# Optimization experiments

Measured on AMD Instinct MI355X. Metric: run time of the kernel, lower is better.

## Reference

```python
import jax, jax.numpy as jnp
import numpy as np
import math

B, S, L, K, NSTEPS = 32, 128, 4096, 129, 10
PAD = K // 2  # torch: int(kernel.shape[-1]/2)


def _grouped_xcorr(x, w):
    # torch F.conv1d semantics (cross-correlation), groups = channels
    # x: [B,C,L] f32, w: [C,1,K] f32 -> [B,C,L]
    return jax.lax.conv_general_dilated(
        x, w, window_strides=(1,), padding=[(PAD, PAD)],
        dimension_numbers=('NCH', 'OIH', 'NCH'), feature_group_count=x.shape[1])


def _matched_filter(x_re, x_im, k_re, k_im):
    # complex grouped conv with conj(kernel) repeated per pulse
    wc_re = jnp.tile(k_re[None, None, :], (S, 1, 1))
    wc_im = jnp.tile(-k_im[None, None, :], (S, 1, 1))  # conj
    out_re = _grouped_xcorr(x_re, wc_re) - _grouped_xcorr(x_im, wc_im)
    out_im = _grouped_xcorr(x_re, wc_im) + _grouped_xcorr(x_im, wc_re)
    return out_re + 1j * out_im  # complex64 [B,S,L]


def _produce_rd(x, w_mag, w_phase):
    phase = jnp.arctan(w_phase)                    # [B,S]
    norm_mag = S * jax.nn.softmax(w_mag, axis=-1)  # [B,S]
    iq = (norm_mag * jnp.exp(-1j * phase))[..., None] * x
    return jnp.fft.fftshift(jnp.fft.fft(iq, axis=-2), axes=-2)


def _circular_weighted_mean(w):
    # circular weighted mean of index over last axis; returns (magnitude, index)
    N = w.shape[-1]
    ang = (2.0 * jnp.pi / N) * jnp.arange(N, dtype=w.dtype)
    z = jnp.sum(w * jnp.exp(1j * ang), axis=-1)
    return jnp.abs(z), jnp.angle(z) / (2.0 * jnp.pi) * N


def _snr(rd):
    Bn, nfft, Ln = rd.shape
    e = jnp.abs(rd) ** 2                                   # [B,S,L]
    flat_idx = jnp.argmax(e.reshape(Bn, -1), axis=1)
    max_range = flat_idx % Ln                              # [B] (indices: constant wrt grad)
    col = jnp.take_along_axis(e, max_range[:, None, None], axis=2)[..., 0]  # [B,S]
    _, peak_idx = _circular_weighted_mean(col)
    # torch rounds + casts to int -> detached index
    idx = jax.lax.stop_gradient(jnp.round(peak_idx)).astype(jnp.int32) % nfft
    peak = jnp.take_along_axis(col, idx[:, None], axis=1)[:, 0]
    noise = (jnp.sum(col, axis=-1) - peak) / (nfft - 1)
    return 10.0 * jnp.log10(peak) - 10.0 * jnp.log10(noise)


def setup_inputs() -> dict:
    key = jax.random.key(0)
    ks = jax.random.split(key, 5)
    return {
        'x_re': jax.random.normal(ks[0], (B, S, L), jnp.float32),
        'x_im': jax.random.normal(ks[1], (B, S, L), jnp.float32),
        'kernel_re': jax.random.normal(ks[2], (K,), jnp.float32),
        'kernel_im': jax.random.normal(ks[3], (K,), jnp.float32),
        'log_step_mag': -2.0 * jnp.ones((S, NSTEPS), jnp.float32),
        'log_step_phase': -2.0 * jnp.ones((S, NSTEPS), jnp.float32),
        'w_phase_init': jax.random.uniform(ks[4], (B, S), jnp.float32),
    }


def reference(x_re, x_im, kernel_re, kernel_im, log_step_mag, log_step_phase, w_phase_init):
    x = _matched_filter(x_re, x_im, kernel_re, kernel_im)  # [B,S,L] complex64
    w_mag = jnp.ones((B, S), jnp.float32)
    w_phase = w_phase_init

    def loss_sum(wm, wp):
        return jnp.sum(_snr(_produce_rd(x, wm, wp)))

    grad_fn = jax.grad(loss_sum, argnums=(0, 1))
    ln10 = math.log(10.0)
    for i in range(NSTEPS):
        # torch detaches w_mag/w_phase before the inner autograd.grad
        g_mag, g_phase = grad_fn(jax.lax.stop_gradient(w_mag),
                                 jax.lax.stop_gradient(w_phase))
        lr_mag = jnp.exp(log_step_mag[:, i] * ln10)    # 10**log_step
        lr_phase = jnp.exp(log_step_phase[:, i] * ln10)
        w_mag = w_mag + lr_mag * g_mag
        w_phase = w_phase + lr_phase * g_phase
    return jnp.mean(_snr(_produce_rd(x, w_mag, w_phase)))
```

## Files before the change

### kernel.cpp

```cpp
#include <hip/hip_runtime.h>

#define BB 32
#define SS 128
#define LL 4096
#define KK 129
#define NST 10

constexpr double PI_D = 3.141592653589793238462643383279502884;
constexpr double red_sin(double x){
  double x2 = x*x, t = x, r = x;
  t *= -x2/6.0;   r += t;
  t *= -x2/20.0;  r += t;
  t *= -x2/42.0;  r += t;
  t *= -x2/72.0;  r += t;
  t *= -x2/110.0; r += t;
  t *= -x2/156.0; r += t;
  t *= -x2/210.0; r += t;
  t *= -x2/272.0; r += t;
  return r;
}
constexpr double csin_d(double x){
  while (x >  PI_D) x -= 2.0*PI_D;
  while (x < -PI_D) x += 2.0*PI_D;
  if (x >  PI_D*0.5)      x =  PI_D - x;
  else if (x < -PI_D*0.5) x = -PI_D - x;
  return red_sin(x);
}
constexpr double ccos_d(double x){ return csin_d(x + PI_D*0.5); }
struct TWT { float c[64]; float s[64]; };
constexpr TWT make_tw(){
  TWT t{};
  for (int j = 0; j < 64; j++){
    double a = -2.0*PI_D*(double)j/128.0;
    t.c[j] = (float)ccos_d(a);
    t.s[j] = (float)csin_d(a);
  }
  return t;
}
constexpr TWT TW = make_tw();

#define PHYS8(i) ((i) + ((i) >> 3))

__global__ __launch_bounds__(256) void mf_kernel(const float* __restrict__ xr,
                                                 const float* __restrict__ xi,
                                                 const float* __restrict__ kr,
                                                 const float* __restrict__ ki,
                                                 float2* __restrict__ out)
{
  const int row = blockIdx.x >> 1;
  const int l0  = (blockIdx.x & 1) * 2048;
  const int t   = threadIdx.x;
  __shared__ float2 xs[2456];
  __shared__ float2 ks[132];
  if (t < KK) ks[t] = make_float2(kr[t], ki[t]);

  const float* xrr = xr + (size_t)row*LL;
  const float* xir = xi + (size_t)row*LL;
  for (int i4 = t; i4 < 544; i4 += 256){
    const int g0 = l0 - 64 + i4*4;
    float4 a, c;
    if (g0 >= 0 && g0 + 3 < LL){
      a = *(const float4*)(xrr + g0);
      c = *(const float4*)(xir + g0);
    } else {
      float av[4], cv[4];
      #pragma unroll
      for (int e = 0; e < 4; ++e){
        const int g = g0 + e;
        const bool ok = (g >= 0 && g < LL);
        av[e] = ok ? xrr[g] : 0.0f;
        cv[e] = ok ? xir[g] : 0.0f;
      }
      a = make_float4(av[0],av[1],av[2],av[3]);
      c = make_float4(cv[0],cv[1],cv[2],cv[3]);
    }
    const int i = i4*4;
    const int p = PHYS8(i);
    xs[p]   = make_float2(a.x, c.x);
    xs[p+1] = make_float2(a.y, c.y);
    xs[p+2] = make_float2(a.z, c.z);
    xs[p+3] = make_float2(a.w, c.w);
  }
  __syncthreads();

  const int base_l = t*8;
  float wr_[16], wi_[16];
  #pragma unroll
  for (int v = 0; v < 12; v += 2){
    const float4 p = *(const float4*)(&xs[PHYS8(base_l + v)]);
    wr_[v]   = p.x; wi_[v]   = p.y;
    wr_[v+1] = p.z; wi_[v+1] = p.w;
  }

  float2 acc[8];
  #pragma unroll
  for (int j = 0; j < 8; j++) acc[j] = make_float2(0.0f, 0.0f);

  #pragma unroll 1
  for (int q8 = 0; q8 < 8; ++q8){
    #pragma unroll
    for (int qq = 0; qq < 4; ++qq){
      const int q = q8*4 + qq;
      float4 p0, p1;
      const bool doref = (q < 31);
      if (doref){
        const int v0 = base_l + q*4 + 12;
        p0 = *(const float4*)(&xs[PHYS8(v0)]);
        p1 = *(const float4*)(&xs[PHYS8(v0 + 2)]);
      }
      float2 wv[4];
      #pragma unroll
      for (int kk = 0; kk < 4; ++kk) wv[kk] = ks[q*4 + kk];
      #pragma unroll
      for (int kk = 0; kk < 4; ++kk){
        const float wx = wv[kk].x, wy = wv[kk].y;
        #pragma unroll
        for (int j = 0; j < 8; ++j){
          const int sl = (qq*4 + kk + j) & 15;
          const float xvr = wr_[sl], xvi = wi_[sl];
          acc[j].x = fmaf(xvr, wx, acc[j].x);
          acc[j].x = fmaf(xvi, wy, acc[j].x);
          acc[j].y = fmaf(xvi, wx, acc[j].y);
          acc[j].y = fmaf(-xvr, wy, acc[j].y);
        }
      }
      if (doref){
        const int s0 = (qq*4 + 12) & 15;
        wr_[s0]   = p0.x; wi_[s0]   = p0.y;
        wr_[s0+1] = p0.z; wi_[s0+1] = p0.w;
        wr_[s0+2] = p1.x; wi_[s0+2] = p1.y;
        wr_[s0+3] = p1.z; wi_[s0+3] = p1.w;
      }
    }
  }
  {
    const float2 w = ks[128];
    #pragma unroll
    for (int j = 0; j < 8; ++j){
      const float xvr = wr_[j], xvi = wi_[j];
      acc[j].x = fmaf(xvr, w.x, acc[j].x);
      acc[j].x = fmaf(xvi, w.y, acc[j].x);
      acc[j].y = fmaf(xvi, w.x, acc[j].y);
      acc[j].y = fmaf(-xvr, w.y, acc[j].y);
    }
  }

  float4* orow = (float4*)(out + (size_t)row*LL + l0 + base_l);
  #pragma unroll
  for (int q = 0; q < 4; ++q){
    orow[q] = make_float4(acc[2*q].x, acc[2*q].y, acc[2*q+1].x, acc[2*q+1].y);
  }
}

__global__ __launch_bounds__(512) void tr_kernel(const float2* __restrict__ xmf,
                                                 float2* __restrict__ xt)
{
  const int b = blockIdx.y;
  const int l0 = blockIdx.x * 64;
  const int tid = threadIdx.x;
  __shared__ float ldr[64][129];
  __shared__ float ldi[64][129];
  #pragma unroll
  for (int it = 0; it < 8; ++it){
    const int flat = it*512 + tid;
    const int s  = flat >> 5;
    const int c4 = flat & 31;
    const float4 p = *(const float4*)(xmf + ((size_t)(b*SS + s))*LL + l0 + 2*c4);
    ldr[2*c4][s]   = p.x;  ldi[2*c4][s]   = p.y;
    ldr[2*c4+1][s] = p.z;  ldi[2*c4+1][s] = p.w;
  }
  __syncthreads();
  #pragma unroll
  for (int it = 0; it < 8; ++it){
    const int flat = it*512 + tid;
    const int dl = flat >> 6;
    const int s4 = flat & 63;
    const float r0 = ldr[dl][2*s4], r1 = ldr[dl][2*s4+1];
    const float i0 = ldi[dl][2*s4], i1 = ldi[dl][2*s4+1];
    *(float4*)(xt + ((size_t)b*LL + l0 + dl)*SS + 2*s4) = make_float4(r0, i0, r1, i1);
  }
}

__global__ void init_kernel(const float* __restrict__ wpi,
                            float* __restrict__ w_mag, float* __restrict__ w_phase,
                            float2* __restrict__ cvec, unsigned long long* __restrict__ slots,
                            float* __restrict__ out)
{
  const int i = blockIdx.x*256 + threadIdx.x;
  if (i < BB*SS){
    float wp = wpi[i];
    w_mag[i] = 1.0f;
    w_phase[i] = wp;
    float phi = atanf(wp);
    float s, c;
    sincosf(phi, &s, &c);
    cvec[i] = make_float2(c, -s);
  }
  if (i < BB) slots[i] = 0ull;
  if (i == 0) out[0] = 0.0f;
}

template<int SPAN, int N>
__device__ __forceinline__ void fstage(float2* v){
  #pragma unroll
  for (int b0 = 0; b0 < N; b0 += 2*SPAN){
    #pragma unroll
    for (int j = 0; j < SPAN; j++){
      const int i0 = b0 + j, i1 = b0 + j + SPAN;
      float ax = v[i0].x, ay = v[i0].y, bx = v[i1].x, by = v[i1].y;
      float sx = ax - bx, sy = ay - by;
      v[i0].x = ax + bx; v[i0].y = ay + by;
      const int tj = j * (64 / SPAN);
      if (tj == 0){
        v[i1].x = sx; v[i1].y = sy;
      } else if (tj == 32){
        v[i1].x = sy; v[i1].y = -sx;
      } else {
        const float wr = TW.c[tj], wi = TW.s[tj];
        v[i1].x = sx*wr - sy*wi;
        v[i1].y = sy*wr + sx*wi;
      }
    }
  }
}

__device__ __forceinline__ void scan_fft_tail(float2* v, int r, int tid, int l,
                                              unsigned long long* wred, int nwave,
                                              unsigned long long* slot)
{
  {
    const bool hi = (r & 2) != 0;
    const float sgn = hi ? -1.0f : 1.0f;
    const bool odd = (r & 1) != 0;
    #pragma unroll
    for (int j = 0; j < 32; ++j){
      float px = __shfl_xor(v[j].x, 2);
      float py = __shfl_xor(v[j].y, 2);
      float ux = fmaf(sgn, v[j].x, px);
      float uy = fmaf(sgn, v[j].y, py);
      float wr = hi ? (odd ? TW.s[j] : TW.c[j]) : 1.0f;
      float wi = hi ? (odd ? -TW.c[j] : TW.s[j]) : 0.0f;
      v[j].x = ux*wr - uy*wi;
      v[j].y = uy*wr + ux*wi;
    }
  }
  {
    const bool hi = (r & 1) != 0;
    const float sgn = hi ? -1.0f : 1.0f;
    #pragma unroll
    for (int j = 0; j < 32; ++j){
      float px = __shfl_xor(v[j].x, 1);
      float py = __shfl_xor(v[j].y, 1);
      float ux = fmaf(sgn, v[j].x, px);
      float uy = fmaf(sgn, v[j].y, py);
      float wr = hi ? TW.c[2*j] : 1.0f;
      float wi = hi ? TW.s[2*j] : 0.0f;
      v[j].x = ux*wr - uy*wi;
      v[j].y = uy*wr + ux*wi;
    }
  }
  fstage<16,32>(v); fstage<8,32>(v); fstage<4,32>(v); fstage<2,32>(v); fstage<1,32>(v);

  float mm = 0.0f;
  #pragma unroll
  for (int j = 0; j < 32; ++j) mm = fmaxf(mm, v[j].x*v[j].x + v[j].y*v[j].y);
  mm = fmaxf(mm, __shfl_xor(mm, 1));
  mm = fmaxf(mm, __shfl_xor(mm, 2));

  unsigned long long pk = ((unsigned long long)__float_as_uint(mm) << 32) | (unsigned int)l;
  #pragma unroll
  for (int m = 4; m < 64; m <<= 1){
    unsigned long long o = __shfl_xor(pk, m);
    if (o > pk) pk = o;
  }
  if ((tid & 63) == 0) wred[tid >> 6] = pk;
  __syncthreads();
  if (tid == 0){
    unsigned long long best = wred[0];
    for (int w = 1; w < nwave; ++w) if (wred[w] > best) best = wred[w];
    atomicMax(slot, best);
  }
}

__global__ __launch_bounds__(256) void scan_t_kernel(const float2* __restrict__ xt,
                                                     const float2* __restrict__ cvec,
                                                     unsigned long long* __restrict__ slots)
{
  const int b = blockIdx.y;
  const int tid = threadIdx.x;
  const int f = tid >> 2, r = tid & 3;
  const int l = blockIdx.x*64 + f;
  __shared__ float2 csh[SS];
  __shared__ unsigned long long wred[4];
  if (tid < SS) csh[tid] = cvec[b*SS + tid];
  __syncthreads();

  const float2* col = xt + ((size_t)b*LL + l)*SS + r*32;
  float2 v[32];
  #pragma unroll
  for (int i = 0; i < 8; ++i){
    const float4 p = ((const float4*)col)[i];
    v[2*i]   = make_float2(p.x, p.y);
    v[2*i+1] = make_float2(p.z, p.w);
  }
  #pragma unroll
  for (int j = 0; j < 32; ++j){
    const float2 c = csh[r*32 + j];
    const float2 x = v[j];
    v[j].x = c.x*x.x - c.y*x.y;
    v[j].y = c.x*x.y + c.y*x.x;
  }
  scan_fft_tail(v, r, tid, l, wred, 4, slots + b);
}

__global__ __launch_bounds__(512, 4) void scan_o_kernel(const float2* __restrict__ xmf,
                                                        const float2* __restrict__ cvec,
                                                        unsigned long long* __restrict__ slots)
{
  const int b = blockIdx.y;
  const int tid = threadIdx.x;
  const int l0 = blockIdx.x * 128;
  __shared__ float2 csh[SS];
  __shared__ float2 xsh[64][130];
  __shared__ unsigned long long wred[8];
  if (tid < SS) csh[tid] = cvec[b*SS + tid];

  const int f = tid >> 2, r = tid & 3;
  float2 v[32];

  #pragma unroll 1
  for (int h = 0; h < 2; ++h){
    __syncthreads();
    const float2* src = xmf + ((size_t)(b*SS + h*64))*LL + l0;
    #pragma unroll
    for (int it = 0; it < 8; ++it){
      const int flat = it*512 + tid;
      const int s1 = flat >> 6;
      const int c4 = flat & 63;
      const float4 vv = *(const float4*)(src + (size_t)s1*LL + c4*2);
      *(float4*)(&xsh[s1][c4*2]) = vv;
    }
    __syncthreads();
    if ((r >> 1) == h){
      #pragma unroll
      for (int j = 0; j < 32; ++j){
        const int rowi = (r & 1)*32 + j;
        const float2 x = xsh[rowi][f];
        const float2 c = csh[r*32 + j];
        v[j].x = c.x*x.x - c.y*x.y;
        v[j].y = c.x*x.y + c.y*x.x;
      }
    }
  }
  scan_fft_tail(v, r, tid, l0 + f, wred, 8, slots + b);
}

__device__ __forceinline__ float wredsum(float v){
  #pragma unroll
  for (int m = 1; m < 64; m <<= 1) v += __shfl_xor(v, m);
  return v;
}
__device__ __forceinline__ float wredmax(float v){
  #pragma unroll
  for (int m = 1; m < 64; m <<= 1) v = fmaxf(v, __shfl_xor(v, m));
  return v;
}
__device__ __forceinline__ float bsum256(float v, float* red4, int t){
  v = wredsum(v);
  __syncthreads();
  if ((t & 63) == 0) red4[t >> 6] = v;
  __syncthreads();
  return red4[0] + red4[1] + red4[2] + red4[3];
}
__device__ __forceinline__ float bmax256(float v, float* red4, int t){
  v = wredmax(v);
  __syncthreads();
  if ((t & 63) == 0) red4[t >> 6] = v;
  __syncthreads();
  return fmaxf(fmaxf(red4[0], red4[1]), fmaxf(red4[2], red4[3]));
}

__global__ __launch_bounds__(256) void step_kernel(const float2* __restrict__ xmf,
                                                   const float2* __restrict__ xt, int useT,
                                                   float* __restrict__ w_mag,
                                                   float* __restrict__ w_phase,
                                                   float2* __restrict__ cvec,
                                                   unsigned long long* __restrict__ slots,
                                                   const float* __restrict__ lsm,
                                                   const float* __restrict__ lsp,
                                                   int stepi, int isFinal,
                                                   float* __restrict__ out)
{
  const int b = blockIdx.x, t = threadIdx.x;
  const int s = t >> 1, h = t & 1;
  __shared__ float2 ysh[SS];
  __shared__ float twc[SS], tws[SS];
  __shared__ float red4[4];
  __shared__ float speak;
  __shared__ int sidx;

  const int rbin = (int)(slots[b] & 0xffffffffull);
  const float wm0 = w_mag[b*SS + s];
  const float wp0 = w_phase[b*SS + s];
  const float2 xc = useT ? xt[((size_t)b*LL + rbin)*SS + s]
                         : xmf[((size_t)(b*SS + s))*LL + rbin];
  float phi = atanf(wp0);
  float sph, cph;
  sincosf(phi, &sph, &cph);
  {
    int id = t & 127;
    float sv, cv;
    sincosf((float)(2.0*PI_D/128.0) * (float)id, &sv, &cv);
    twc[id] = cv; tws[id] = -sv;
  }
  float mx = bmax256(wm0, red4, t);
  float ex = expf(wm0 - mx);
  float sm = bsum256(ex, red4, t) * 0.5f;
  float m = 128.0f * ex / sm;
  float cre = m*cph, cim = -m*sph;
  ysh[s] = make_float2(cre*xc.x - cim*xc.y, cre*xc.y + cim*xc.x);
  __syncthreads();

  const int k = s;
  float Fr = 0.0f, Fi = 0.0f;
  #pragma unroll 8
  for (int q = 0; q < 64; ++q){
    int s2 = h*64 + q;
    int id = (k*s2) & 127;
    float wr = twc[id], wi = tws[id];
    float2 ys = ysh[s2];
    Fr += wr*ys.x - wi*ys.y;
    Fi += wr*ys.y + wi*ys.x;
  }
  Fr += __shfl_xor(Fr, 1);
  Fi += __shfl_xor(Fi, 1);
  const int u = (k + 64) & 127;
  float colu = Fr*Fr + Fi*Fi;

  float total = bsum256(colu, red4, t) * 0.5f;
  float zre = bsum256(colu * twc[u], red4, t) * 0.5f;
  float zim = bsum256(colu * (-tws[u]), red4, t) * 0.5f;
  if (t == 0){
    float ang = atan2f(zim, zre);
    float pidx = ang * (128.0f/(2.0f*(float)PI_D));
    sidx = ((int)rintf(pidx)) & 127;
  }
  __syncthreads();
  const int idx = sidx;
  if (u == idx && h == 0) speak = colu;
  __syncthreads();
  const float peak = speak;
  const float noise = (total - peak) * (1.0f/127.0f);

  if (isFinal){
    if (t == 0) atomicAdd(out, 10.0f*(log10f(peak) - log10f(noise)) * (1.0f/(float)BB));
    return;
  }

  constexpr float C10 = 4.342944819032518f;
  float g = (u == idx) ? (C10/peak) : (-C10/(127.0f*noise));
  __syncthreads();
  ysh[k] = make_float2(2.0f*g*Fr, 2.0f*g*Fi);
  __syncthreads();

  float Tr = 0.0f, Ti = 0.0f;
  #pragma unroll 8
  for (int q = 0; q < 64; ++q){
    int kk = h*64 + q;
    int id = (s*kk) & 127;
    float wr = twc[id], wi = -tws[id];
    float2 G = ysh[kk];
    Tr += wr*G.x - wi*G.y;
    Ti += wr*G.y + wi*G.x;
  }
  Tr += __shfl_xor(Tr, 1);
  Ti += __shfl_xor(Ti, 1);

  float Hr = xc.x*Tr + xc.y*Ti;
  float Hi = xc.x*Ti - xc.y*Tr;
  float dm   = Hr*cph - Hi*sph;
  float dphi = -m*(Hr*sph + Hi*cph);
  float S1 = bsum256(m*dm, red4, t) * 0.5f;
  float gwm = m*(dm - S1*(1.0f/128.0f));
  float gwp = dphi / (1.0f + wp0*wp0);

  constexpr float LN10 = 2.302585092994046f;
  float lrm = expf(lsm[s*NST + stepi] * LN10);
  float lrp = expf(lsp[s*NST + stepi] * LN10);
  float wm1 = wm0 + lrm*gwm;
  float wp1 = wp0 + lrp*gwp;
  if (h == 0){
    w_mag[b*SS + s] = wm1;
    w_phase[b*SS + s] = wp1;
  }

  float mx2 = bmax256(wm1, red4, t);
  float ex2 = expf(wm1 - mx2);
  float sm2 = bsum256(ex2, red4, t) * 0.5f;
  float m2 = 128.0f * ex2 / sm2;
  float phi2 = atanf(wp1);
  float s2v, c2v;
  sincosf(phi2, &s2v, &c2v);
  if (h == 0) cvec[b*SS + s] = make_float2(m2*c2v, -m2*s2v);
  if (t == 0) slots[b] = 0ull;
}

extern "C" void kernel_launch(void* const* d_in, const int* in_sizes, int n_in,
                              void* d_out, int out_size, void* d_ws, size_t ws_size,
                              hipStream_t stream)
{
  const float* x_re = (const float*)d_in[0];
  const float* x_im = (const float*)d_in[1];
  const float* k_re = (const float*)d_in[2];
  const float* k_im = (const float*)d_in[3];
  const float* lsm  = (const float*)d_in[4];
  const float* lsp  = (const float*)d_in[5];
  const float* wpi  = (const float*)d_in[6];
  float* out = (float*)d_out;

  char* ws = (char*)d_ws;
  size_t off = 0;
  float2* xmf = (float2*)(ws + off);                 off += (size_t)BB*SS*LL*sizeof(float2);
  unsigned long long* slots = (unsigned long long*)(ws + off); off += 256;
  float* w_mag   = (float*)(ws + off);               off += (size_t)BB*SS*4;
  float* w_phase = (float*)(ws + off);               off += (size_t)BB*SS*4;
  float2* cvec   = (float2*)(ws + off);              off += (size_t)BB*SS*8;
  const size_t off_base = off;
  float2* xt = (float2*)(ws + off);                  off += (size_t)BB*SS*LL*sizeof(float2);
  const int useT = (ws_size >= off) ? 1 : 0;
  if (ws_size < off_base) return;

  mf_kernel<<<BB*SS*2, 256, 0, stream>>>(x_re, x_im, k_re, k_im, xmf);
  init_kernel<<<(BB*SS + 255)/256, 256, 0, stream>>>(wpi, w_mag, w_phase, cvec, slots, out);
  if (useT) tr_kernel<<<dim3(LL/64, BB), 512, 0, stream>>>(xmf, xt);

  for (int i = 0; i < NST; i++){
    if (useT) scan_t_kernel<<<dim3(LL/64, BB), 256, 0, stream>>>(xt, cvec, slots);
    else      scan_o_kernel<<<dim3(LL/128, BB), 512, 0, stream>>>(xmf, cvec, slots);
    step_kernel<<<BB, 256, 0, stream>>>(xmf, xt, useT, w_mag, w_phase, cvec, slots, lsm, lsp, i, 0, out);
  }
  if (useT) scan_t_kernel<<<dim3(LL/64, BB), 256, 0, stream>>>(xt, cvec, slots);
  else      scan_o_kernel<<<dim3(LL/128, BB), 512, 0, stream>>>(xmf, cvec, slots);
  step_kernel<<<BB, 256, 0, stream>>>(xmf, xt, useT, w_mag, w_phase, cvec, slots, lsm, lsp, 0, 1, out);
}
```

Measured before the change: 808.9 us.

## Store transposed pulse data in wave-coalesced float4 layout for scan kernel

The transpose kernel now writes the pulse-major copy in a custom interleaved layout where each wavefront's per-iteration float4 loads are contiguous across lanes. Previously each thread in the scan kernel read a 256-byte strided column chunk, which gave poorly coalesced loads. The shared-memory tile is re-swizzled to stay free of bank conflicts under the new read pattern. The step kernel no longer reads from the transposed buffer and always gathers from the original matched-filter output.

After: 795.9 us. Within noise of the previous version (-1.6%).

```diff
diff --git a/kernel.cpp b/kernel.cpp
--- a/kernel.cpp
+++ b/kernel.cpp
@@ -153,31 +153,36 @@
 }
 
 __global__ __launch_bounds__(512) void tr_kernel(const float2* __restrict__ xmf,
-                                                 float2* __restrict__ xt)
+                                                 float4* __restrict__ xt2)
 {
   const int b = blockIdx.y;
   const int l0 = blockIdx.x * 64;
   const int tid = threadIdx.x;
-  __shared__ float ldr[64][129];
-  __shared__ float ldi[64][129];
+  __shared__ float ldr[SS][65];
+  __shared__ float ldi[SS][65];
   #pragma unroll
   for (int it = 0; it < 8; ++it){
     const int flat = it*512 + tid;
     const int s  = flat >> 5;
     const int c4 = flat & 31;
     const float4 p = *(const float4*)(xmf + ((size_t)(b*SS + s))*LL + l0 + 2*c4);
-    ldr[2*c4][s]   = p.x;  ldi[2*c4][s]   = p.y;
-    ldr[2*c4+1][s] = p.z;  ldi[2*c4+1][s] = p.w;
-  }
-  __syncthreads();
+    const int sw = 8*(s >> 5);
+    ldr[s][(2*c4   + sw) & 63] = p.x;  ldi[s][(2*c4   + sw) & 63] = p.y;
+    ldr[s][(2*c4+1 + sw) & 63] = p.z;  ldi[s][(2*c4+1 + sw) & 63] = p.w;
+  }
+  __syncthreads();
+  float4* dst = xt2 + ((size_t)(b*256 + blockIdx.x*4) * 16) * 64;
   #pragma unroll
   for (int it = 0; it < 8; ++it){
     const int flat = it*512 + tid;
-    const int dl = flat >> 6;
-    const int s4 = flat & 63;
-    const float r0 = ldr[dl][2*s4], r1 = ldr[dl][2*s4+1];
-    const float i0 = ldi[dl][2*s4], i1 = ldi[dl][2*s4+1];
-    *(float4*)(xt + ((size_t)b*LL + l0 + dl)*SS + 2*s4) = make_float4(r0, i0, r1, i1);
+    const int lane = flat & 63;
+    const int i   = (flat >> 6) & 15;
+    const int lgl = flat >> 10;
+    const int fl = lane >> 2, r = lane & 3;
+    const int lrow = lgl*16 + fl;
+    const int s0 = r*32 + 2*i;
+    const int col = (lrow + 8*r) & 63;
+    dst[flat] = make_float4(ldr[s0][col], ldi[s0][col], ldr[s0+1][col], ldi[s0+1][col]);
   }
 }
 
@@ -282,7 +287,7 @@
   }
 }
 
-__global__ __launch_bounds__(256) void scan_t_kernel(const float2* __restrict__ xt,
+__global__ __launch_bounds__(256) void scan_t_kernel(const float4* __restrict__ xt2,
                                                      const float2* __restrict__ cvec,
                                                      unsigned long long* __restrict__ slots)
 {
@@ -290,16 +295,18 @@
   const int tid = threadIdx.x;
   const int f = tid >> 2, r = tid & 3;
   const int l = blockIdx.x*64 + f;
+  const int w = tid >> 6;
+  const int lg = blockIdx.x*4 + w;
   __shared__ float2 csh[SS];
   __shared__ unsigned long long wred[4];
   if (tid < SS) csh[tid] = cvec[b*SS + tid];
   __syncthreads();
 
-  const float2* col = xt + ((size_t)b*LL + l)*SS + r*32;
+  const float4* base = xt2 + ((size_t)(b*(LL/16) + lg) * 16) * 64 + (tid & 63);
   float2 v[32];
   #pragma unroll
-  for (int i = 0; i < 8; ++i){
-    const float4 p = ((const float4*)col)[i];
+  for (int i = 0; i < 16; ++i){
+    const float4 p = base[i*64];
     v[2*i]   = make_float2(p.x, p.y);
     v[2*i+1] = make_float2(p.z, p.w);
   }
@@ -381,7 +388,6 @@
 }
 
 __global__ __launch_bounds__(256) void step_kernel(const float2* __restrict__ xmf,
-                                                   const float2* __restrict__ xt, int useT,
                                                    float* __restrict__ w_mag,
                                                    float* __restrict__ w_phase,
                                                    float2* __restrict__ cvec,
@@ -402,8 +408,7 @@
   const int rbin = (int)(slots[b] & 0xffffffffull);
   const float wm0 = w_mag[b*SS + s];
   const float wp0 = w_phase[b*SS + s];
-  const float2 xc = useT ? xt[((size_t)b*LL + rbin)*SS + s]
-                         : xmf[((size_t)(b*SS + s))*LL + rbin];
+  const float2 xc = xmf[((size_t)(b*SS + s))*LL + rbin];
   float phi = atanf(wp0);
   float sph, cph;
   sincosf(phi, &sph, &cph);
@@ -526,20 +531,20 @@
   float* w_phase = (float*)(ws + off);               off += (size_t)BB*SS*4;
   float2* cvec   = (float2*)(ws + off);              off += (size_t)BB*SS*8;
   const size_t off_base = off;
-  float2* xt = (float2*)(ws + off);                  off += (size_t)BB*SS*LL*sizeof(float2);
+  float4* xt2 = (float4*)(ws + off);                 off += (size_t)BB*SS*LL*sizeof(float2);
   const int useT = (ws_size >= off) ? 1 : 0;
   if (ws_size < off_base) return;
 
   mf_kernel<<<BB*SS*2, 256, 0, stream>>>(x_re, x_im, k_re, k_im, xmf);
   init_kernel<<<(BB*SS + 255)/256, 256, 0, stream>>>(wpi, w_mag, w_phase, cvec, slots, out);
-  if (useT) tr_kernel<<<dim3(LL/64, BB), 512, 0, stream>>>(xmf, xt);
+  if (useT) tr_kernel<<<dim3(LL/64, BB), 512, 0, stream>>>(xmf, xt2);
 
   for (int i = 0; i < NST; i++){
-    if (useT) scan_t_kernel<<<dim3(LL/64, BB), 256, 0, stream>>>(xt, cvec, slots);
+    if (useT) scan_t_kernel<<<dim3(LL/64, BB), 256, 0, stream>>>(xt2, cvec, slots);
     else      scan_o_kernel<<<dim3(LL/128, BB), 512, 0, stream>>>(xmf, cvec, slots);
-    step_kernel<<<BB, 256, 0, stream>>>(xmf, xt, useT, w_mag, w_phase, cvec, slots, lsm, lsp, i, 0, out);
-  }
-  if (useT) scan_t_kernel<<<dim3(LL/64, BB), 256, 0, stream>>>(xt, cvec, slots);
+    step_kernel<<<BB, 256, 0, stream>>>(xmf, w_mag, w_phase, cvec, slots, lsm, lsp, i, 0, out);
+  }
+  if (useT) scan_t_kernel<<<dim3(LL/64, BB), 256, 0, stream>>>(xt2, cvec, slots);
   else      scan_o_kernel<<<dim3(LL/128, BB), 512, 0, stream>>>(xmf, cvec, slots);
-  step_kernel<<<BB, 256, 0, stream>>>(xmf, xt, useT, w_mag, w_phase, cvec, slots, lsm, lsp, 0, 1, out);
-}
+  step_kernel<<<BB, 256, 0, stream>>>(xmf, w_mag, w_phase, cvec, slots, lsm, lsp, 0, 1, out);
+}
```
